# Kernel tuning notes

Measured on AMD Instinct MI355X. Metric: run time of the kernel, lower is better.

## Reference

```python
import jax, jax.numpy as jnp
import numpy as np

ALPHA = 0.2  # LeakyReLU negative slope
NEG = -9e15

def _gat_head(Wh, a1, a2, adj_mask):
    # Wh: [N,O], a1/a2: [O], adj_mask: [N,N] bool
    e = jax.nn.leaky_relu(jnp.einsum('no,o->n', Wh, a1)[:, None]
                          + jnp.einsum('no,o->n', Wh, a2)[None, :], ALPHA)
    att = jax.nn.softmax(jnp.where(adj_mask, e, NEG), axis=-1)
    return att @ Wh  # [N,O]

def setup_inputs() -> dict:
    key = jax.random.key(0)
    ks = jax.random.split(key, 6)
    N, F_IN, O, H, C = 4096, 512, 64, 8, 16
    x = jax.random.normal(ks[0], (N, F_IN), jnp.float32)
    adj = jax.random.randint(ks[1], (N, N), 0, 2, jnp.int32)
    W = jax.random.normal(ks[2], (H, F_IN, O), jnp.float32) * 0.05
    a = jax.random.normal(ks[3], (H, 2 * O), jnp.float32) * 0.05
    W_out = jax.random.normal(ks[4], (H * O, C), jnp.float32) * 0.05
    a_out = jax.random.normal(ks[5], (2 * C,), jnp.float32) * 0.05
    return {'x': x, 'adj': adj, 'W': W, 'a': a, 'W_out': W_out, 'a_out': a_out}

def reference(x, adj, W, a, W_out, a_out):
    N = x.shape[0]
    H, _, O = W.shape
    C = W_out.shape[1]
    mask = adj > 0  # [N,N]
    # multi-head attention layer (vmapped over heads)
    Wh = jnp.einsum('nf,hfo->hno', x, W)  # [H,N,O]
    a1, a2 = a[:, :O], a[:, O:]
    h_heads = jax.vmap(_gat_head, in_axes=(0, 0, 0, None))(Wh, a1, a2, mask)  # [H,N,O]
    h = jax.nn.elu(h_heads)  # concat=True -> elu per head
    h = jnp.transpose(h, (1, 0, 2)).reshape(N, H * O)  # concat heads
    # output attention layer (concat=False)
    Wh_o = h @ W_out  # [N,C]
    out = _gat_head(Wh_o, a_out[:C], a_out[C:], mask)  # [N,C]
    out = jax.nn.elu(out)
    return jax.nn.log_softmax(out, axis=1)
```

## Files before the change

### kernel.cpp

```cpp
#include <hip/hip_runtime.h>


typedef __attribute__((ext_vector_type(8))) short short8;
typedef __attribute__((ext_vector_type(4))) float f32x4;
typedef unsigned long long u64;
typedef unsigned short u16;

__device__ __forceinline__ u16 f2bf_rne(float f){
  unsigned int u = __float_as_uint(f);
  return (u16)((u + 0x7fffu + ((u >> 16) & 1u)) >> 16);
}
__device__ __forceinline__ float bf2f(u16 v){
  return __uint_as_float(((unsigned int)v) << 16);
}
__device__ __forceinline__ void async16(void* lds, const void* g){
  __builtin_amdgcn_global_load_lds((const __attribute__((address_space(1))) unsigned int*)g,
                                   (__attribute__((address_space(3))) unsigned int*)lds, 16, 0, 0);
}
__device__ __forceinline__ void async4(void* lds, const void* g){
  __builtin_amdgcn_global_load_lds((const __attribute__((address_space(1))) unsigned int*)g,
                                   (__attribute__((address_space(3))) unsigned int*)lds, 4, 0, 0);
}

__global__ __launch_bounds__(256) void k_adj_pack(const int* __restrict__ adj,
                                                  u64* __restrict__ bits){
  int lane = threadIdx.x & 63;
  int w0 = blockIdx.x * 4 + (threadIdx.x >> 6);
  #pragma unroll
  for (int k = 0; k < 16; ++k){
    int wid = w0 + k * 16384;
    int i  = wid >> 6;
    int jg = wid & 63;
    int v = adj[(size_t)i * 4096 + (jg << 6) + lane];
    u64 m = __ballot(v != 0);
    if (lane == 0) bits[(size_t)i * 64 + jg] = m;
  }
}

__global__ __launch_bounds__(256) void k_pack_in(const float* __restrict__ x,
                                                 const float* __restrict__ W,
                                                 u16* __restrict__ xA,
                                                 u16* __restrict__ wB){
  if (blockIdx.x < 1024){
    int tid = blockIdx.x * 256 + threadIdx.x;
    int n = tid & 4095;
    int fg = tid >> 12;
    const float* src = x + (size_t)n * 512 + fg * 8;
    float4 v0 = ((const float4*)src)[0];
    float4 v1 = ((const float4*)src)[1];
    unsigned int pk[4];
    pk[0] = f2bf_rne(v0.x) | ((unsigned)f2bf_rne(v0.y) << 16);
    pk[1] = f2bf_rne(v0.z) | ((unsigned)f2bf_rne(v0.w) << 16);
    pk[2] = f2bf_rne(v1.x) | ((unsigned)f2bf_rne(v1.y) << 16);
    pk[3] = f2bf_rne(v1.z) | ((unsigned)f2bf_rne(v1.w) << 16);
    *(uint4*)(xA + ((size_t)fg * 4096 + n) * 8) = *(uint4*)pk;
  } else {
    int tid = (blockIdx.x - 1024) * 256 + threadIdx.x;
    int o  = tid & 63;
    int fg = (tid >> 6) & 63;
    int h  = tid >> 12;
    const float* src = W + ((size_t)h * 512 + fg * 8) * 64 + o;
    unsigned int pk[4];
    #pragma unroll
    for (int p = 0; p < 4; ++p){
      u16 lo = f2bf_rne(src[(2 * p) * 64]);
      u16 hi = f2bf_rne(src[(2 * p + 1) * 64]);
      pk[p] = lo | ((unsigned)hi << 16);
    }
    *(uint4*)(wB + (size_t)h * 32768 + ((size_t)fg * 64 + o) * 8) = *(uint4*)pk;
  }
}

__global__ __launch_bounds__(256) void k_gemm1(const u16* __restrict__ xA,
                                               const u16* __restrict__ wB,
                                               float* __restrict__ Whf){
  int h    = blockIdx.y;
  int nblk = blockIdx.x;
  int lane = threadIdx.x & 63;
  int wid  = threadIdx.x >> 6;
  int row16 = lane & 15, grp = lane >> 4;
  int n0 = nblk * 64 + wid * 16;
  const u16* wBh = wB + (size_t)h * 32768;
  f32x4 acc[4] = {};
  #pragma unroll 4
  for (int ks = 0; ks < 16; ++ks){
    int fgb = ks * 4 + grp;
    short8 af = *(const short8*)(xA + ((size_t)fgb * 4096 + n0 + row16) * 8);
    #pragma unroll
    for (int nt = 0; nt < 4; ++nt){
      short8 bf = *(const short8*)(wBh + ((size_t)fgb * 64 + nt * 16 + row16) * 8);
      acc[nt] = __builtin_amdgcn_mfma_f32_16x16x32_bf16(af, bf, acc[nt], 0, 0, 0);
    }
  }
  #pragma unroll
  for (int nt = 0; nt < 4; ++nt)
    #pragma unroll
    for (int r = 0; r < 4; ++r){
      int n = n0 + grp * 4 + r;
      int o = nt * 16 + row16;
      Whf[((size_t)h * 4096 + n) * 64 + o] = acc[nt][r];
    }
}

__global__ __launch_bounds__(256) void k_prep1(const float* __restrict__ Whf,
                                               const float* __restrict__ av,
                                               u16* __restrict__ whB,
                                               float* __restrict__ s1raw, float* __restrict__ e11,
                                               float* __restrict__ e102, float* __restrict__ s2raw,
                                               float* __restrict__ e21, float* __restrict__ e202){
  if (blockIdx.x < 1024){
    int tid = blockIdx.x * 256 + threadIdx.x;
    int o  = tid & 63;
    int jg = (tid >> 6) & 511;
    int h  = tid >> 15;
    const float* src = Whf + ((size_t)h * 4096 + jg * 8) * 64 + o;
    unsigned int pk[4];
    #pragma unroll
    for (int p = 0; p < 4; ++p){
      u16 lo = f2bf_rne(src[(2 * p) * 64]);
      u16 hi = f2bf_rne(src[(2 * p + 1) * 64]);
      pk[p] = lo | ((unsigned)hi << 16);
    }
    *(uint4*)(whB + (size_t)h * 262144 + ((size_t)jg * 64 + o) * 8) = *(uint4*)pk;
  } else {
    int lane = threadIdx.x & 63;
    int wid  = (blockIdx.x - 1024) * 4 + (threadIdx.x >> 6);
    int h = wid >> 12;
    int i = wid & 4095;
    float wh = Whf[((size_t)h * 4096 + i) * 64 + lane];
    float p1 = wh * av[h * 128 + lane];
    float p2 = wh * av[h * 128 + 64 + lane];
    #pragma unroll
    for (int d = 32; d; d >>= 1){ p1 += __shfl_xor(p1, d, 64); p2 += __shfl_xor(p2, d, 64); }
    if (lane == 0){
      int idx = h * 4096 + i;
      s1raw[idx] = p1; e11[idx] = __expf(p1); e102[idx] = __expf(0.2f * p1);
      s2raw[idx] = p2; e21[idx] = __expf(p2); e202[idx] = __expf(0.2f * p2);
    }
  }
}

__global__ __launch_bounds__(256) void k_att1(const u16* __restrict__ whB,
                                              const u64* __restrict__ adjbits,
                                              const float* __restrict__ s1raw, const float* __restrict__ e11,
                                              const float* __restrict__ e102, const float* __restrict__ s2raw,
                                              const float* __restrict__ e21, const float* __restrict__ e202,
                                              u16* __restrict__ pnum, float* __restrict__ pden){
  __shared__ u16  smB[2][8 * 520];
  __shared__ float smT[2][3][64];
  int h     = blockIdx.y;
  int iblk  = blockIdx.x;
  int split = blockIdx.z;
  int lane = threadIdx.x & 63;
  int wid  = threadIdx.x >> 6;
  int row16 = lane & 15, grp = lane >> 4;
  int i = iblk * 64 + wid * 16 + row16;
  int hoff = h * 4096;
  float s1  = s1raw[hoff + i];
  float f1  = e11[hoff + i];
  float f02 = e102[hoff + i];
  const u16* whBh = whB + (size_t)h * 262144;
  int jbeg = split * 1024;

  auto stage = [&](int b, int j0){
    const char* g = (const char*)whBh + (size_t)j0 * 128 + wid * 2048 + lane * 16;
    char* l = (char*)(&smB[b][0]) + wid * 2 * 1040;
    async16(l, g);
    async16(l + 1040, g + 1024);
    if (wid == 0)      async4(&smT[b][0][0], (const char*)(s2raw + hoff + j0) + lane * 4);
    else if (wid == 1) async4(&smT[b][1][0], (const char*)(e21  + hoff + j0) + lane * 4);
    else if (wid == 2) async4(&smT[b][2][0], (const char*)(e202 + hoff + j0) + lane * 4);
  };

  f32x4 acc[4] = {};
  float den = 0.f;
  stage(0, jbeg);
  for (int c = 0; c < 16; ++c){
    int b = c & 1;
    __syncthreads();
    if (c < 15) stage(b ^ 1, jbeg + (c + 1) * 64);
    u64 mrow = adjbits[(size_t)i * 64 + ((jbeg + c * 64) >> 6)];
    #pragma unroll
    for (int ks = 0; ks < 2; ++ks){
      int kb = ks * 32 + grp * 8;
      float4 sA = *(const float4*)(&smT[b][0][kb]);
      float4 sB = *(const float4*)(&smT[b][0][kb + 4]);
      float4 eA = *(const float4*)(&smT[b][1][kb]);
      float4 eB = *(const float4*)(&smT[b][1][kb + 4]);
      float4 gA = *(const float4*)(&smT[b][2][kb]);
      float4 gB2 = *(const float4*)(&smT[b][2][kb + 4]);
      float sv[8]  = {sA.x, sA.y, sA.z, sA.w, sB.x, sB.y, sB.z, sB.w};
      float e1v[8] = {eA.x, eA.y, eA.z, eA.w, eB.x, eB.y, eB.z, eB.w};
      float e2v[8] = {gA.x, gA.y, gA.z, gA.w, gB2.x, gB2.y, gB2.z, gB2.w};
      unsigned int mb = ((unsigned int)(mrow >> (ks * 32)) >> (grp * 8)) & 0xffu;
      unsigned int pk[4];
      #pragma unroll
      for (int t2 = 0; t2 < 4; ++t2){
        float w0, w1;
        {
          float tt = s1 + sv[2 * t2];
          float w = (tt > 0.f) ? (f1 * e1v[2 * t2]) : (f02 * e2v[2 * t2]);
          w = ((mb >> (2 * t2)) & 1u) ? w : 0.f;
          den += w; w0 = w;
        }
        {
          float tt = s1 + sv[2 * t2 + 1];
          float w = (tt > 0.f) ? (f1 * e1v[2 * t2 + 1]) : (f02 * e2v[2 * t2 + 1]);
          w = ((mb >> (2 * t2 + 1)) & 1u) ? w : 0.f;
          den += w; w1 = w;
        }
        pk[t2] = __builtin_amdgcn_perm(__float_as_uint(w1), __float_as_uint(w0), 0x07060302u);
      }
      short8 af = *(short8*)pk;
      const u16* bbase = &smB[b][(ks * 4 + grp) * 520];
      #pragma unroll
      for (int nt = 0; nt < 4; ++nt){
        short8 bf = *(const short8*)(bbase + (nt * 16 + row16) * 8);
        acc[nt] = __builtin_amdgcn_mfma_f32_16x16x32_bf16(af, bf, acc[nt], 0, 0, 0);
      }
    }
  }

  den += __shfl_xor(den, 16, 64);
  den += __shfl_xor(den, 32, 64);
  if (grp == 0)
    pden[((size_t)split * 8 + h) * 4096 + iblk * 64 + wid * 16 + row16] = den;
  #pragma unroll
  for (int r = 0; r < 4; ++r){
    int n = iblk * 64 + wid * 16 + grp * 4 + r;
    u16* dst = pnum + ((size_t)split * 4096 + n) * 512 + h * 64 + row16;
    #pragma unroll
    for (int nt = 0; nt < 4; ++nt)
      dst[nt * 16] = f2bf_rne(acc[nt][r]);
  }
}

__global__ __launch_bounds__(256) void k_gemm2(const u16* __restrict__ pnum,
                                               const float* __restrict__ pden,
                                               const float* __restrict__ Wout,
                                               const float* __restrict__ aout,
                                               u16* __restrict__ whoB,
                                               float* __restrict__ s1o, float* __restrict__ e11o,
                                               float* __restrict__ e102o, float* __restrict__ s2o,
                                               float* __restrict__ e21o, float* __restrict__ e202o){
  __shared__ float Wl[8192];
  __shared__ float hrow[16 * 516];
  __shared__ float sden[128];
  int n0 = blockIdx.x * 16;
  for (int t = threadIdx.x; t < 8192; t += 256) Wl[t] = Wout[t];
  if (threadIdx.x < 128){
    int hh = threadIdx.x >> 4, nn = threadIdx.x & 15;
    float d = 0.f;
    #pragma unroll
    for (int s = 0; s < 4; ++s) d += pden[((size_t)s * 8 + hh) * 4096 + n0 + nn];
    sden[threadIdx.x] = d;
  }
  __syncthreads();
  {
    int nn = threadIdx.x >> 4;
    int fc = threadIdx.x & 15;
    int f0 = fc * 32;
    int hh = fc >> 1;
    float dinv = 1.f / sden[hh * 16 + nn];
    float v[32];
    #pragma unroll
    for (int k = 0; k < 32; ++k) v[k] = 0.f;
    #pragma unroll
    for (int s = 0; s < 4; ++s){
      const u16* p = pnum + ((size_t)s * 4096 + n0 + nn) * 512 + f0;
      #pragma unroll
      for (int q = 0; q < 4; ++q){
        uint4 raw = *(const uint4*)(p + q * 8);
        unsigned int rw[4] = {raw.x, raw.y, raw.z, raw.w};
        #pragma unroll
        for (int d2 = 0; d2 < 4; ++d2){
          v[q * 8 + d2 * 2]     += __uint_as_float(rw[d2] << 16);
          v[q * 8 + d2 * 2 + 1] += __uint_as_float(rw[d2] & 0xffff0000u);
        }
      }
    }
    #pragma unroll
    for (int k = 0; k < 32; ++k){
      float val = v[k] * dinv;
      val = val > 0.f ? val : (__expf(val) - 1.f);
      hrow[nn * 516 + f0 + k] = val;
    }
  }
  __syncthreads();
  int c  = threadIdx.x & 15;
  int rl = threadIdx.x >> 4;
  int n = n0 + rl;
  const float4* hr = (const float4*)(hrow + rl * 516);
  float acc = 0.f;
  #pragma unroll 8
  for (int f4 = 0; f4 < 128; ++f4){
    float4 hv = hr[f4];
    int f = f4 * 4;
    acc += hv.x * Wl[f * 16 + c] + hv.y * Wl[(f + 1) * 16 + c]
         + hv.z * Wl[(f + 2) * 16 + c] + hv.w * Wl[(f + 3) * 16 + c];
  }
  whoB[((size_t)(n >> 3) * 16 + c) * 8 + (n & 7)] = f2bf_rne(acc);
  float p1 = acc * aout[c], p2 = acc * aout[16 + c];
  #pragma unroll
  for (int d = 1; d < 16; d <<= 1){ p1 += __shfl_xor(p1, d, 64); p2 += __shfl_xor(p2, d, 64); }
  if (c == 0){
    s1o[n] = p1; e11o[n] = __expf(p1); e102o[n] = __expf(0.2f * p1);
    s2o[n] = p2; e21o[n] = __expf(p2); e202o[n] = __expf(0.2f * p2);
  }
}

__global__ __launch_bounds__(256) void k_att2(const u16* __restrict__ whoB,
                                              const u64* __restrict__ adjbits,
                                              const float* __restrict__ s1o, const float* __restrict__ e11o,
                                              const float* __restrict__ e102o, const float* __restrict__ s2o,
                                              const float* __restrict__ e21o, const float* __restrict__ e202o,
                                              float* __restrict__ pnum, float* __restrict__ pden){
  __shared__ u16  smB[2][1024];
  __shared__ float smT[2][3][64];
  int iblk  = blockIdx.x;
  int split = blockIdx.y;
  int lane = threadIdx.x & 63;
  int wid  = threadIdx.x >> 6;
  int row16 = lane & 15, grp = lane >> 4;
  int i = iblk * 64 + wid * 16 + row16;
  float s1  = s1o[i];
  float f1  = e11o[i];
  float f02 = e102o[i];
  int jbeg = split * 256;

  auto stage = [&](int b, int j0){
    const char* gB = (const char*)whoB + (size_t)j0 * 32;
    if (wid == 0){
      async16((char*)&smB[b][0], gB + lane * 16);
      async16((char*)&smB[b][0] + 1024, gB + 1024 + lane * 16);
    }
    else if (wid == 1) async4(&smT[b][0][0], (const char*)(s2o  + j0) + lane * 4);
    else if (wid == 2) async4(&smT[b][1][0], (const char*)(e21o + j0) + lane * 4);
    else               async4(&smT[b][2][0], (const char*)(e202o + j0) + lane * 4);
  };

  f32x4 acc = {};
  float den = 0.f;
  stage(0, jbeg);
  for (int c = 0; c < 4; ++c){
    int b = c & 1;
    __syncthreads();
    if (c < 3) stage(b ^ 1, jbeg + (c + 1) * 64);
    u64 mrow = adjbits[(size_t)i * 64 + ((jbeg + c * 64) >> 6)];
    #pragma unroll
    for (int ks = 0; ks < 2; ++ks){
      int kb = ks * 32 + grp * 8;
      float4 sA = *(const float4*)(&smT[b][0][kb]);
      float4 sB = *(const float4*)(&smT[b][0][kb + 4]);
      float4 eA = *(const float4*)(&smT[b][1][kb]);
      float4 eB = *(const float4*)(&smT[b][1][kb + 4]);
      float4 gA = *(const float4*)(&smT[b][2][kb]);
      float4 gB2 = *(const float4*)(&smT[b][2][kb + 4]);
      float sv[8]  = {sA.x, sA.y, sA.z, sA.w, sB.x, sB.y, sB.z, sB.w};
      float e1v[8] = {eA.x, eA.y, eA.z, eA.w, eB.x, eB.y, eB.z, eB.w};
      float e2v[8] = {gA.x, gA.y, gA.z, gA.w, gB2.x, gB2.y, gB2.z, gB2.w};
      unsigned int mb = ((unsigned int)(mrow >> (ks * 32)) >> (grp * 8)) & 0xffu;
      unsigned int pk[4];
      #pragma unroll
      for (int t2 = 0; t2 < 4; ++t2){
        float w0, w1;
        {
          float tt = s1 + sv[2 * t2];
          float w = (tt > 0.f) ? (f1 * e1v[2 * t2]) : (f02 * e2v[2 * t2]);
          w = ((mb >> (2 * t2)) & 1u) ? w : 0.f;
          den += w; w0 = w;
        }
        {
          float tt = s1 + sv[2 * t2 + 1];
          float w = (tt > 0.f) ? (f1 * e1v[2 * t2 + 1]) : (f02 * e2v[2 * t2 + 1]);
          w = ((mb >> (2 * t2 + 1)) & 1u) ? w : 0.f;
          den += w; w1 = w;
        }
        pk[t2] = __builtin_amdgcn_perm(__float_as_uint(w1), __float_as_uint(w0), 0x07060302u);
      }
      short8 af = *(short8*)pk;
      short8 bf = *(const short8*)(&smB[b][((ks * 4 + grp) * 16 + row16) * 8]);
      acc = __builtin_amdgcn_mfma_f32_16x16x32_bf16(af, bf, acc, 0, 0, 0);
    }
  }
  den += __shfl_xor(den, 16, 64);
  den += __shfl_xor(den, 32, 64);
  if (grp == 0)
    pden[(size_t)(iblk * 64 + wid * 16 + row16) * 16 + split] = den;
  #pragma unroll
  for (int r = 0; r < 4; ++r){
    int n = iblk * 64 + wid * 16 + grp * 4 + r;
    pnum[((size_t)n * 16 + split) * 16 + row16] = acc[r];
  }
}

__global__ __launch_bounds__(256) void k_final(const float* __restrict__ pnum,
                                               const float* __restrict__ pden,
                                               float* __restrict__ out){
  int tid = blockIdx.x * 256 + threadIdx.x;
  int c = tid & 15;
  int n = tid >> 4;
  float num = 0.f, den = 0.f;
  #pragma unroll
  for (int s = 0; s < 16; ++s){
    num += pnum[((size_t)n * 16 + s) * 16 + c];
    den += pden[(size_t)n * 16 + s];
  }
  float v = num / den;
  v = v > 0.f ? v : (__expf(v) - 1.f);
  float m = v;
  #pragma unroll
  for (int d = 1; d < 16; d <<= 1) m = fmaxf(m, __shfl_xor(m, d, 64));
  float es = __expf(v - m), ss = es;
  #pragma unroll
  for (int d = 1; d < 16; d <<= 1) ss += __shfl_xor(ss, d, 64);
  out[(size_t)n * 16 + c] = v - m - __logf(ss);
}

extern "C" void kernel_launch(void* const* d_in, const int* in_sizes, int n_in,
                              void* d_out, int out_size, void* d_ws, size_t ws_size,
                              hipStream_t stream){
  (void)in_sizes; (void)n_in; (void)out_size; (void)ws_size;
  const float* x    = (const float*)d_in[0];
  const int*   adj  = (const int*)d_in[1];
  const float* W    = (const float*)d_in[2];
  const float* av   = (const float*)d_in[3];
  const float* Wout = (const float*)d_in[4];
  const float* aout = (const float*)d_in[5];
  float* out = (float*)d_out;
  char* ws = (char*)d_ws;

  u64*  adjbits = (u64*)(ws + 0x0000000);
  u16*  whB     = (u16*)(ws + 0x0200000);
  float* s1raw  = (float*)(ws + 0x0600000);
  float* e11    = (float*)(ws + 0x0620000);
  float* e102   = (float*)(ws + 0x0640000);
  float* s2raw  = (float*)(ws + 0x0660000);
  float* e21    = (float*)(ws + 0x0680000);
  float* e202   = (float*)(ws + 0x06A0000);
  u16*  xA   = (u16*)(ws + 0x06C0000);
  float* Whf = (float*)(ws + 0x0AC0000);
  u16*  wB   = (u16*)(ws + 0x12C0000);
  u16*  pnum1 = (u16*)(ws + 0x06C0000);
  float* pden1 = (float*)(ws + 0x16C0000);
  u16*  whoB   = (u16*)(ws + 0x1740000);
  float* s1o   = (float*)(ws + 0x1760000);
  float* e11o  = (float*)(ws + 0x1764000);
  float* e102o = (float*)(ws + 0x1768000);
  float* s2o   = (float*)(ws + 0x176C000);
  float* e21o  = (float*)(ws + 0x1770000);
  float* e202o = (float*)(ws + 0x1774000);
  float* pnum2 = (float*)(ws + 0x1778000);
  float* pden2 = (float*)(ws + 0x1B78000);

  k_adj_pack<<<dim3(4096), dim3(256), 0, stream>>>(adj, adjbits);
  k_pack_in<<<dim3(1152), dim3(256), 0, stream>>>(x, W, xA, wB);
  k_gemm1<<<dim3(64, 8), dim3(256), 0, stream>>>(xA, wB, Whf);
  k_prep1<<<dim3(9216), dim3(256), 0, stream>>>(Whf, av, whB, s1raw, e11, e102, s2raw, e21, e202);
  k_att1<<<dim3(64, 8, 4), dim3(256), 0, stream>>>(whB, adjbits, s1raw, e11, e102, s2raw, e21, e202, pnum1, pden1);
  k_gemm2<<<dim3(256), dim3(256), 0, stream>>>(pnum1, pden1, Wout, aout, whoB, s1o, e11o, e102o, s2o, e21o, e202o);
  k_att2<<<dim3(64, 16), dim3(256), 0, stream>>>(whoB, adjbits, s1o, e11o, e102o, s2o, e21o, e202o, pnum2, pden2);
  k_final<<<dim3(256), dim3(256), 0, stream>>>(pnum2, pden2, out);
}
```

Baseline: 208.1 us.

## Fuse prep into GEMM1, compute attention weights via max, denominator via MFMA

Folds the score-dot and bf16 transpose-pack of k_prep1 into k_gemm1's epilogue through LDS, which removes the fp32 Wh round trip and one launch. The attention kernels replace the LeakyReLU sign branch with fmaxf of the two exponential products, which works because exp is monotonic. Masking now uses an LDS lookup-table AND, and the row denominator comes from an extra MFMA against a ones column instead of scalar adds. k_att1 handles 128 rows per block, two row tiles per wave, so each B fragment loaded from LDS is reused. The unpadded LDS layout may add bank conflicts, and the denominator now sums bf16-rounded weights, which costs some precision.

```diff
diff --git a/kernel.cpp b/kernel.cpp
--- a/kernel.cpp
+++ b/kernel.cpp
@@ -5,21 +5,19 @@
 typedef __attribute__((ext_vector_type(4))) float f32x4;
 typedef unsigned long long u64;
 typedef unsigned short u16;
+typedef unsigned int u32;
 
 __device__ __forceinline__ u16 f2bf_rne(float f){
-  unsigned int u = __float_as_uint(f);
+  u32 u = __float_as_uint(f);
   return (u16)((u + 0x7fffu + ((u >> 16) & 1u)) >> 16);
 }
-__device__ __forceinline__ float bf2f(u16 v){
-  return __uint_as_float(((unsigned int)v) << 16);
-}
 __device__ __forceinline__ void async16(void* lds, const void* g){
-  __builtin_amdgcn_global_load_lds((const __attribute__((address_space(1))) unsigned int*)g,
-                                   (__attribute__((address_space(3))) unsigned int*)lds, 16, 0, 0);
+  __builtin_amdgcn_global_load_lds((const __attribute__((address_space(1))) u32*)g,
+                                   (__attribute__((address_space(3))) u32*)lds, 16, 0, 0);
 }
 __device__ __forceinline__ void async4(void* lds, const void* g){
-  __builtin_amdgcn_global_load_lds((const __attribute__((address_space(1))) unsigned int*)g,
-                                   (__attribute__((address_space(3))) unsigned int*)lds, 4, 0, 0);
+  __builtin_amdgcn_global_load_lds((const __attribute__((address_space(1))) u32*)g,
+                                   (__attribute__((address_space(3))) u32*)lds, 4, 0, 0);
 }
 
 __global__ __launch_bounds__(256) void k_adj_pack(const int* __restrict__ adj,
@@ -48,11 +46,11 @@
     const float* src = x + (size_t)n * 512 + fg * 8;
     float4 v0 = ((const float4*)src)[0];
     float4 v1 = ((const float4*)src)[1];
-    unsigned int pk[4];
-    pk[0] = f2bf_rne(v0.x) | ((unsigned)f2bf_rne(v0.y) << 16);
-    pk[1] = f2bf_rne(v0.z) | ((unsigned)f2bf_rne(v0.w) << 16);
-    pk[2] = f2bf_rne(v1.x) | ((unsigned)f2bf_rne(v1.y) << 16);
-    pk[3] = f2bf_rne(v1.z) | ((unsigned)f2bf_rne(v1.w) << 16);
+    u32 pk[4];
+    pk[0] = f2bf_rne(v0.x) | ((u32)f2bf_rne(v0.y) << 16);
+    pk[1] = f2bf_rne(v0.z) | ((u32)f2bf_rne(v0.w) << 16);
+    pk[2] = f2bf_rne(v1.x) | ((u32)f2bf_rne(v1.y) << 16);
+    pk[3] = f2bf_rne(v1.z) | ((u32)f2bf_rne(v1.w) << 16);
     *(uint4*)(xA + ((size_t)fg * 4096 + n) * 8) = *(uint4*)pk;
   } else {
     int tid = (blockIdx.x - 1024) * 256 + threadIdx.x;
@@ -60,12 +58,12 @@
     int fg = (tid >> 6) & 63;
     int h  = tid >> 12;
     const float* src = W + ((size_t)h * 512 + fg * 8) * 64 + o;
-    unsigned int pk[4];
+    u32 pk[4];
     #pragma unroll
     for (int p = 0; p < 4; ++p){
       u16 lo = f2bf_rne(src[(2 * p) * 64]);
       u16 hi = f2bf_rne(src[(2 * p + 1) * 64]);
-      pk[p] = lo | ((unsigned)hi << 16);
+      pk[p] = lo | ((u32)hi << 16);
     }
     *(uint4*)(wB + (size_t)h * 32768 + ((size_t)fg * 64 + o) * 8) = *(uint4*)pk;
   }
@@ -73,165 +71,159 @@
 
 __global__ __launch_bounds__(256) void k_gemm1(const u16* __restrict__ xA,
                                                const u16* __restrict__ wB,
-                                               float* __restrict__ Whf){
+                                               const float* __restrict__ av,
+                                               u16* __restrict__ whB,
+                                               float* __restrict__ e11, float* __restrict__ e102,
+                                               float* __restrict__ e21, float* __restrict__ e202){
+  __shared__ u16 tr[4096];
   int h    = blockIdx.y;
   int nblk = blockIdx.x;
   int lane = threadIdx.x & 63;
   int wid  = threadIdx.x >> 6;
   int row16 = lane & 15, grp = lane >> 4;
-  int n0 = nblk * 64 + wid * 16;
+  int n0 = nblk * 64;
+  int n0w = n0 + wid * 16;
   const u16* wBh = wB + (size_t)h * 32768;
   f32x4 acc[4] = {};
   #pragma unroll 4
   for (int ks = 0; ks < 16; ++ks){
     int fgb = ks * 4 + grp;
-    short8 af = *(const short8*)(xA + ((size_t)fgb * 4096 + n0 + row16) * 8);
+    short8 af = *(const short8*)(xA + ((size_t)fgb * 4096 + n0w + row16) * 8);
     #pragma unroll
     for (int nt = 0; nt < 4; ++nt){
       short8 bf = *(const short8*)(wBh + ((size_t)fgb * 64 + nt * 16 + row16) * 8);
       acc[nt] = __builtin_amdgcn_mfma_f32_16x16x32_bf16(af, bf, acc[nt], 0, 0, 0);
     }
   }
+  float a1v[4], a2v[4];
+  #pragma unroll
+  for (int nt = 0; nt < 4; ++nt){
+    a1v[nt] = av[h * 128 + nt * 16 + row16];
+    a2v[nt] = av[h * 128 + 64 + nt * 16 + row16];
+  }
+  #pragma unroll
+  for (int r = 0; r < 4; ++r){
+    float p1 = acc[0][r] * a1v[0] + acc[1][r] * a1v[1] + acc[2][r] * a1v[2] + acc[3][r] * a1v[3];
+    float p2 = acc[0][r] * a2v[0] + acc[1][r] * a2v[1] + acc[2][r] * a2v[2] + acc[3][r] * a2v[3];
+    #pragma unroll
+    for (int d = 1; d < 16; d <<= 1){ p1 += __shfl_xor(p1, d, 64); p2 += __shfl_xor(p2, d, 64); }
+    if (row16 == 0){
+      int idx = h * 4096 + n0w + grp * 4 + r;
+      e11[idx]  = __expf(p1); e102[idx] = __expf(0.2f * p1);
+      e21[idx]  = __expf(p2); e202[idx] = __expf(0.2f * p2);
+    }
+  }
   #pragma unroll
   for (int nt = 0; nt < 4; ++nt)
     #pragma unroll
     for (int r = 0; r < 4; ++r){
-      int n = n0 + grp * 4 + r;
-      int o = nt * 16 + row16;
-      Whf[((size_t)h * 4096 + n) * 64 + o] = acc[nt][r];
-    }
-}
-
-__global__ __launch_bounds__(256) void k_prep1(const float* __restrict__ Whf,
-                                               const float* __restrict__ av,
-                                               u16* __restrict__ whB,
-                                               float* __restrict__ s1raw, float* __restrict__ e11,
-                                               float* __restrict__ e102, float* __restrict__ s2raw,
-                                               float* __restrict__ e21, float* __restrict__ e202){
-  if (blockIdx.x < 1024){
-    int tid = blockIdx.x * 256 + threadIdx.x;
-    int o  = tid & 63;
-    int jg = (tid >> 6) & 511;
-    int h  = tid >> 15;
-    const float* src = Whf + ((size_t)h * 4096 + jg * 8) * 64 + o;
-    unsigned int pk[4];
-    #pragma unroll
-    for (int p = 0; p < 4; ++p){
-      u16 lo = f2bf_rne(src[(2 * p) * 64]);
-      u16 hi = f2bf_rne(src[(2 * p + 1) * 64]);
-      pk[p] = lo | ((unsigned)hi << 16);
-    }
-    *(uint4*)(whB + (size_t)h * 262144 + ((size_t)jg * 64 + o) * 8) = *(uint4*)pk;
-  } else {
-    int lane = threadIdx.x & 63;
-    int wid  = (blockIdx.x - 1024) * 4 + (threadIdx.x >> 6);
-    int h = wid >> 12;
-    int i = wid & 4095;
-    float wh = Whf[((size_t)h * 4096 + i) * 64 + lane];
-    float p1 = wh * av[h * 128 + lane];
-    float p2 = wh * av[h * 128 + 64 + lane];
-    #pragma unroll
-    for (int d = 32; d; d >>= 1){ p1 += __shfl_xor(p1, d, 64); p2 += __shfl_xor(p2, d, 64); }
-    if (lane == 0){
-      int idx = h * 4096 + i;
-      s1raw[idx] = p1; e11[idx] = __expf(p1); e102[idx] = __expf(0.2f * p1);
-      s2raw[idx] = p2; e21[idx] = __expf(p2); e202[idx] = __expf(0.2f * p2);
-    }
-  }
+      int jl = wid * 16 + grp * 4 + r;
+      int o  = nt * 16 + row16;
+      tr[((jl >> 3) * 64 + o) * 8 + (jl & 7)] = f2bf_rne(acc[nt][r]);
+    }
+  __syncthreads();
+  u16* dst = whB + (size_t)h * 262144 + (size_t)n0 * 64;
+  #pragma unroll
+  for (int q = 0; q < 2; ++q)
+    *(uint4*)(dst + (threadIdx.x * 2 + q) * 8) = *(const uint4*)(tr + (threadIdx.x * 2 + q) * 8);
 }
 
 __global__ __launch_bounds__(256) void k_att1(const u16* __restrict__ whB,
                                               const u64* __restrict__ adjbits,
-                                              const float* __restrict__ s1raw, const float* __restrict__ e11,
-                                              const float* __restrict__ e102, const float* __restrict__ s2raw,
+                                              const float* __restrict__ e11, const float* __restrict__ e102,
                                               const float* __restrict__ e21, const float* __restrict__ e202,
                                               u16* __restrict__ pnum, float* __restrict__ pden){
-  __shared__ u16  smB[2][8 * 520];
-  __shared__ float smT[2][3][64];
+  __shared__ u16  smB[2][4096];
+  __shared__ float smT[2][2][64];
+  __shared__ u32  smLut[4];
   int h     = blockIdx.y;
   int iblk  = blockIdx.x;
   int split = blockIdx.z;
   int lane = threadIdx.x & 63;
   int wid  = threadIdx.x >> 6;
   int row16 = lane & 15, grp = lane >> 4;
-  int i = iblk * 64 + wid * 16 + row16;
+  if (threadIdx.x < 4)
+    smLut[threadIdx.x] = ((threadIdx.x & 1) ? 0xFFFFu : 0u) | ((threadIdx.x & 2) ? 0xFFFF0000u : 0u);
+  int ibase = iblk * 128 + wid * 32;
+  int i0 = ibase + row16, i1 = ibase + 16 + row16;
   int hoff = h * 4096;
-  float s1  = s1raw[hoff + i];
-  float f1  = e11[hoff + i];
-  float f02 = e102[hoff + i];
+  float f1a  = e11[hoff + i0],  f1b  = e11[hoff + i1];
+  float f02a = e102[hoff + i0], f02b = e102[hoff + i1];
   const u16* whBh = whB + (size_t)h * 262144;
   int jbeg = split * 1024;
 
+  short8 bden;
+  #pragma unroll
+  for (int t = 0; t < 8; ++t) bden[t] = (row16 == 0) ? (short)0x3F80 : (short)0;
+
   auto stage = [&](int b, int j0){
     const char* g = (const char*)whBh + (size_t)j0 * 128 + wid * 2048 + lane * 16;
-    char* l = (char*)(&smB[b][0]) + wid * 2 * 1040;
+    char* l = (char*)(&smB[b][0]) + wid * 2048;
     async16(l, g);
-    async16(l + 1040, g + 1024);
-    if (wid == 0)      async4(&smT[b][0][0], (const char*)(s2raw + hoff + j0) + lane * 4);
-    else if (wid == 1) async4(&smT[b][1][0], (const char*)(e21  + hoff + j0) + lane * 4);
-    else if (wid == 2) async4(&smT[b][2][0], (const char*)(e202 + hoff + j0) + lane * 4);
+    async16(l + 1024, g + 1024);
+    if (wid == 0)      async4(&smT[b][0][0], (const char*)(e21  + hoff + j0) + lane * 4);
+    else if (wid == 1) async4(&smT[b][1][0], (const char*)(e202 + hoff + j0) + lane * 4);
   };
 
-  f32x4 acc[4] = {};
-  float den = 0.f;
+  f32x4 acc[2][4] = {};
+  f32x4 accden[2] = {};
   stage(0, jbeg);
   for (int c = 0; c < 16; ++c){
     int b = c & 1;
+    u64 mrow0 = adjbits[(size_t)i0 * 64 + ((jbeg + c * 64) >> 6)];
+    u64 mrow1 = adjbits[(size_t)i1 * 64 + ((jbeg + c * 64) >> 6)];
     __syncthreads();
     if (c < 15) stage(b ^ 1, jbeg + (c + 1) * 64);
-    u64 mrow = adjbits[(size_t)i * 64 + ((jbeg + c * 64) >> 6)];
     #pragma unroll
     for (int ks = 0; ks < 2; ++ks){
       int kb = ks * 32 + grp * 8;
-      float4 sA = *(const float4*)(&smT[b][0][kb]);
-      float4 sB = *(const float4*)(&smT[b][0][kb + 4]);
-      float4 eA = *(const float4*)(&smT[b][1][kb]);
-      float4 eB = *(const float4*)(&smT[b][1][kb + 4]);
-      float4 gA = *(const float4*)(&smT[b][2][kb]);
-      float4 gB2 = *(const float4*)(&smT[b][2][kb + 4]);
-      float sv[8]  = {sA.x, sA.y, sA.z, sA.w, sB.x, sB.y, sB.z, sB.w};
+      float4 eA = *(const float4*)(&smT[b][0][kb]);
+      float4 eB = *(const float4*)(&smT[b][0][kb + 4]);
+      float4 gA = *(const float4*)(&smT[b][1][kb]);
+      float4 gB = *(const float4*)(&smT[b][1][kb + 4]);
       float e1v[8] = {eA.x, eA.y, eA.z, eA.w, eB.x, eB.y, eB.z, eB.w};
-      float e2v[8] = {gA.x, gA.y, gA.z, gA.w, gB2.x, gB2.y, gB2.z, gB2.w};
-      unsigned int mb = ((unsigned int)(mrow >> (ks * 32)) >> (grp * 8)) & 0xffu;
-      unsigned int pk[4];
+      float e2v[8] = {gA.x, gA.y, gA.z, gA.w, gB.x, gB.y, gB.z, gB.w};
+      const u16* bbase = &smB[b][(ks * 4 + grp) * 512];
+      short8 bf0 = *(const short8*)(bbase + (0 * 16 + row16) * 8);
+      short8 bf1 = *(const short8*)(bbase + (1 * 16 + row16) * 8);
+      short8 bf2 = *(const short8*)(bbase + (2 * 16 + row16) * 8);
+      short8 bf3 = *(const short8*)(bbase + (3 * 16 + row16) * 8);
       #pragma unroll
-      for (int t2 = 0; t2 < 4; ++t2){
-        float w0, w1;
-        {
-          float tt = s1 + sv[2 * t2];
-          float w = (tt > 0.f) ? (f1 * e1v[2 * t2]) : (f02 * e2v[2 * t2]);
-          w = ((mb >> (2 * t2)) & 1u) ? w : 0.f;
-          den += w; w0 = w;
+      for (int it = 0; it < 2; ++it){
+        u64 mrow = it ? mrow1 : mrow0;
+        float f1 = it ? f1b : f1a;
+        float f02 = it ? f02b : f02a;
+        u32 mb = ((u32)(mrow >> (ks * 32)) >> (grp * 8)) & 0xffu;
+        u32 pk[4];
+        #pragma unroll
+        for (int t2 = 0; t2 < 4; ++t2){
+          float w0 = fmaxf(f1 * e1v[2 * t2],     f02 * e2v[2 * t2]);
+          float w1 = fmaxf(f1 * e1v[2 * t2 + 1], f02 * e2v[2 * t2 + 1]);
+          u32 p = __builtin_amdgcn_perm(__float_as_uint(w1), __float_as_uint(w0), 0x07060302u);
+          pk[t2] = p & smLut[(mb >> (2 * t2)) & 3u];
         }
-        {
-          float tt = s1 + sv[2 * t2 + 1];
-          float w = (tt > 0.f) ? (f1 * e1v[2 * t2 + 1]) : (f02 * e2v[2 * t2 + 1]);
-          w = ((mb >> (2 * t2 + 1)) & 1u) ? w : 0.f;
-          den += w; w1 = w;
-        }
-        pk[t2] = __builtin_amdgcn_perm(__float_as_uint(w1), __float_as_uint(w0), 0x07060302u);
+        short8 af = *(short8*)pk;
+        acc[it][0] = __builtin_amdgcn_mfma_f32_16x16x32_bf16(af, bf0, acc[it][0], 0, 0, 0);
+        acc[it][1] = __builtin_amdgcn_mfma_f32_16x16x32_bf16(af, bf1, acc[it][1], 0, 0, 0);
+        acc[it][2] = __builtin_amdgcn_mfma_f32_16x16x32_bf16(af, bf2, acc[it][2], 0, 0, 0);
+        acc[it][3] = __builtin_amdgcn_mfma_f32_16x16x32_bf16(af, bf3, acc[it][3], 0, 0, 0);
+        accden[it] = __builtin_amdgcn_mfma_f32_16x16x32_bf16(af, bden, accden[it], 0, 0, 0);
       }
-      short8 af = *(short8*)pk;
-      const u16* bbase = &smB[b][(ks * 4 + grp) * 520];
+    }
+  }
+
+  #pragma unroll
+  for (int it = 0; it < 2; ++it){
+    #pragma unroll
+    for (int r = 0; r < 4; ++r){
+      int n = ibase + it * 16 + grp * 4 + r;
+      if (row16 == 0)
+        pden[((size_t)split * 8 + h) * 4096 + n] = accden[it][r];
+      u16* dst = pnum + ((size_t)split * 4096 + n) * 512 + h * 64 + row16;
       #pragma unroll
-      for (int nt = 0; nt < 4; ++nt){
-        short8 bf = *(const short8*)(bbase + (nt * 16 + row16) * 8);
-        acc[nt] = __builtin_amdgcn_mfma_f32_16x16x32_bf16(af, bf, acc[nt], 0, 0, 0);
-      }
-    }
-  }
-
-  den += __shfl_xor(den, 16, 64);
-  den += __shfl_xor(den, 32, 64);
-  if (grp == 0)
-    pden[((size_t)split * 8 + h) * 4096 + iblk * 64 + wid * 16 + row16] = den;
-  #pragma unroll
-  for (int r = 0; r < 4; ++r){
-    int n = iblk * 64 + wid * 16 + grp * 4 + r;
-    u16* dst = pnum + ((size_t)split * 4096 + n) * 512 + h * 64 + row16;
-    #pragma unroll
-    for (int nt = 0; nt < 4; ++nt)
-      dst[nt * 16] = f2bf_rne(acc[nt][r]);
+      for (int nt = 0; nt < 4; ++nt)
+        dst[nt * 16] = f2bf_rne(acc[it][nt][r]);
+    }
   }
 }
 
@@ -240,8 +232,7 @@
                                                const float* __restrict__ Wout,
                                                const float* __restrict__ aout,
                                                u16* __restrict__ whoB,
-                                               float* __restrict__ s1o, float* __restrict__ e11o,
-                                               float* __restrict__ e102o, float* __restrict__ s2o,
+                                               float* __restrict__ e11o, float* __restrict__ e102o,
                                                float* __restrict__ e21o, float* __restrict__ e202o){
   __shared__ float Wl[8192];
   __shared__ float hrow[16 * 516];
@@ -271,7 +262,7 @@
       #pragma unroll
       for (int q = 0; q < 4; ++q){
         uint4 raw = *(const uint4*)(p + q * 8);
-        unsigned int rw[4] = {raw.x, raw.y, raw.z, raw.w};
+        u32 rw[4] = {raw.x, raw.y, raw.z, raw.w};
         #pragma unroll
         for (int d2 = 0; d2 < 4; ++d2){
           v[q * 8 + d2 * 2]     += __uint_as_float(rw[d2] << 16);
@@ -304,29 +295,33 @@
   #pragma unroll
   for (int d = 1; d < 16; d <<= 1){ p1 += __shfl_xor(p1, d, 64); p2 += __shfl_xor(p2, d, 64); }
   if (c == 0){
-    s1o[n] = p1; e11o[n] = __expf(p1); e102o[n] = __expf(0.2f * p1);
-    s2o[n] = p2; e21o[n] = __expf(p2); e202o[n] = __expf(0.2f * p2);
+    e11o[n] = __expf(p1); e102o[n] = __expf(0.2f * p1);
+    e21o[n] = __expf(p2); e202o[n] = __expf(0.2f * p2);
   }
 }
 
 __global__ __launch_bounds__(256) void k_att2(const u16* __restrict__ whoB,
                                               const u64* __restrict__ adjbits,
-                                              const float* __restrict__ s1o, const float* __restrict__ e11o,
-                                              const float* __restrict__ e102o, const float* __restrict__ s2o,
+                                              const float* __restrict__ e11o, const float* __restrict__ e102o,
                                               const float* __restrict__ e21o, const float* __restrict__ e202o,
                                               float* __restrict__ pnum, float* __restrict__ pden){
   __shared__ u16  smB[2][1024];
-  __shared__ float smT[2][3][64];
+  __shared__ float smT[2][2][64];
+  __shared__ u32  smLut[4];
   int iblk  = blockIdx.x;
   int split = blockIdx.y;
   int lane = threadIdx.x & 63;
   int wid  = threadIdx.x >> 6;
   int row16 = lane & 15, grp = lane >> 4;
+  if (threadIdx.x < 4)
+    smLut[threadIdx.x] = ((threadIdx.x & 1) ? 0xFFFFu : 0u) | ((threadIdx.x & 2) ? 0xFFFF0000u : 0u);
   int i = iblk * 64 + wid * 16 + row16;
-  float s1  = s1o[i];
   float f1  = e11o[i];
   float f02 = e102o[i];
   int jbeg = split * 256;
+  short8 bden;
+  #pragma unroll
+  for (int t = 0; t < 8; ++t) bden[t] = (row16 == 0) ? (short)0x3F80 : (short)0;
 
   auto stage = [&](int b, int j0){
     const char* gB = (const char*)whoB + (size_t)j0 * 32;
@@ -334,62 +329,47 @@
       async16((char*)&smB[b][0], gB + lane * 16);
       async16((char*)&smB[b][0] + 1024, gB + 1024 + lane * 16);
     }
-    else if (wid == 1) async4(&smT[b][0][0], (const char*)(s2o  + j0) + lane * 4);
-    else if (wid == 2) async4(&smT[b][1][0], (const char*)(e21o + j0) + lane * 4);
-    else               async4(&smT[b][2][0], (const char*)(e202o + j0) + lane * 4);
+    else if (wid == 1) async4(&smT[b][0][0], (const char*)(e21o  + j0) + lane * 4);
+    else if (wid == 2) async4(&smT[b][1][0], (const char*)(e202o + j0) + lane * 4);
   };
 
   f32x4 acc = {};
-  float den = 0.f;
+  f32x4 accden = {};
   stage(0, jbeg);
   for (int c = 0; c < 4; ++c){
     int b = c & 1;
+    u64 mrow = adjbits[(size_t)i * 64 + ((jbeg + c * 64) >> 6)];
     __syncthreads();
     if (c < 3) stage(b ^ 1, jbeg + (c + 1) * 64);
-    u64 mrow = adjbits[(size_t)i * 64 + ((jbeg + c * 64) >> 6)];
     #pragma unroll
     for (int ks = 0; ks < 2; ++ks){
       int kb = ks * 32 + grp * 8;
-      float4 sA = *(const float4*)(&smT[b][0][kb]);
-      float4 sB = *(const float4*)(&smT[b][0][kb + 4]);
-      float4 eA = *(const float4*)(&smT[b][1][kb]);
-      float4 eB = *(const float4*)(&smT[b][1][kb + 4]);
-      float4 gA = *(const float4*)(&smT[b][2][kb]);
-      float4 gB2 = *(const float4*)(&smT[b][2][kb + 4]);
-      float sv[8]  = {sA.x, sA.y, sA.z, sA.w, sB.x, sB.y, sB.z, sB.w};
+      float4 eA = *(const float4*)(&smT[b][0][kb]);
+      float4 eB = *(const float4*)(&smT[b][0][kb + 4]);
+      float4 gA = *(const float4*)(&smT[b][1][kb]);
+      float4 gB = *(const float4*)(&smT[b][1][kb + 4]);
       float e1v[8] = {eA.x, eA.y, eA.z, eA.w, eB.x, eB.y, eB.z, eB.w};
-      float e2v[8] = {gA.x, gA.y, gA.z, gA.w, gB2.x, gB2.y, gB2.z, gB2.w};
-      unsigned int mb = ((unsigned int)(mrow >> (ks * 32)) >> (grp * 8)) & 0xffu;
-      unsigned int pk[4];
+      float e2v[8] = {gA.x, gA.y, gA.z, gA.w, gB.x, gB.y, gB.z, gB.w};
+      u32 mb = ((u32)(mrow >> (ks * 32)) >> (grp * 8)) & 0xffu;
+      u32 pk[4];
       #pragma unroll
       for (int t2 = 0; t2 < 4; ++t2){
-        float w0, w1;
-        {
-          float tt = s1 + sv[2 * t2];
-          float w = (tt > 0.f) ? (f1 * e1v[2 * t2]) : (f02 * e2v[2 * t2]);
-          w = ((mb >> (2 * t2)) & 1u) ? w : 0.f;
-          den += w; w0 = w;
-        }
-        {
-          float tt = s1 + sv[2 * t2 + 1];
-          float w = (tt > 0.f) ? (f1 * e1v[2 * t2 + 1]) : (f02 * e2v[2 * t2 + 1]);
-          w = ((mb >> (2 * t2 + 1)) & 1u) ? w : 0.f;
-          den += w; w1 = w;
-        }
-        pk[t2] = __builtin_amdgcn_perm(__float_as_uint(w1), __float_as_uint(w0), 0x07060302u);
+        float w0 = fmaxf(f1 * e1v[2 * t2],     f02 * e2v[2 * t2]);
+        float w1 = fmaxf(f1 * e1v[2 * t2 + 1], f02 * e2v[2 * t2 + 1]);
+        u32 p = __builtin_amdgcn_perm(__float_as_uint(w1), __float_as_uint(w0), 0x07060302u);
+        pk[t2] = p & smLut[(mb >> (2 * t2)) & 3u];
       }
       short8 af = *(short8*)pk;
       short8 bf = *(const short8*)(&smB[b][((ks * 4 + grp) * 16 + row16) * 8]);
-      acc = __builtin_amdgcn_mfma_f32_16x16x32_bf16(af, bf, acc, 0, 0, 0);
-    }
-  }
-  den += __shfl_xor(den, 16, 64);
-  den += __shfl_xor(den, 32, 64);
-  if (grp == 0)
-    pden[(size_t)(iblk * 64 + wid * 16 + row16) * 16 + split] = den;
+      acc    = __builtin_amdgcn_mfma_f32_16x16x32_bf16(af, bf, acc, 0, 0, 0);
+      accden = __builtin_amdgcn_mfma_f32_16x16x32_bf16(af, bden, accden, 0, 0, 0);
+    }
+  }
   #pragma unroll
   for (int r = 0; r < 4; ++r){
     int n = iblk * 64 + wid * 16 + grp * 4 + r;
+    if (row16 == 0)
+      pden[(size_t)n * 16 + split] = accden[r];
     pnum[((size_t)n * 16 + split) * 16 + row16] = acc[r];
   }
 }
@@ -432,33 +412,27 @@
 
   u64*  adjbits = (u64*)(ws + 0x0000000);
   u16*  whB     = (u16*)(ws + 0x0200000);
-  float* s1raw  = (float*)(ws + 0x0600000);
-  float* e11    = (float*)(ws + 0x0620000);
-  float* e102   = (float*)(ws + 0x0640000);
-  float* s2raw  = (float*)(ws + 0x0660000);
-  float* e21    = (float*)(ws + 0x0680000);
-  float* e202   = (float*)(ws + 0x06A0000);
-  u16*  xA   = (u16*)(ws + 0x06C0000);
-  float* Whf = (float*)(ws + 0x0AC0000);
-  u16*  wB   = (u16*)(ws + 0x12C0000);
-  u16*  pnum1 = (u16*)(ws + 0x06C0000);
-  float* pden1 = (float*)(ws + 0x16C0000);
-  u16*  whoB   = (u16*)(ws + 0x1740000);
-  float* s1o   = (float*)(ws + 0x1760000);
-  float* e11o  = (float*)(ws + 0x1764000);
-  float* e102o = (float*)(ws + 0x1768000);
-  float* s2o   = (float*)(ws + 0x176C000);
-  float* e21o  = (float*)(ws + 0x1770000);
-  float* e202o = (float*)(ws + 0x1774000);
-  float* pnum2 = (float*)(ws + 0x1778000);
-  float* pden2 = (float*)(ws + 0x1B78000);
+  float* e11    = (float*)(ws + 0x0600000);
+  float* e102   = (float*)(ws + 0x0620000);
+  float* e21    = (float*)(ws + 0x0640000);
+  float* e202   = (float*)(ws + 0x0660000);
+  u16*  xA    = (u16*)(ws + 0x0680000);
+  u16*  wB    = (u16*)(ws + 0x0A80000);
+  u16*  pnum1 = (u16*)(ws + 0x0680000);
+  float* pden1 = (float*)(ws + 0x1680000);
+  u16*  whoB   = (u16*)(ws + 0x1700000);
+  float* e11o  = (float*)(ws + 0x1720000);
+  float* e102o = (float*)(ws + 0x1724000);
+  float* e21o  = (float*)(ws + 0x1728000);
+  float* e202o = (float*)(ws + 0x172C000);
+  float* pnum2 = (float*)(ws + 0x1730000);
+  float* pden2 = (float*)(ws + 0x1B30000);
 
   k_adj_pack<<<dim3(4096), dim3(256), 0, stream>>>(adj, adjbits);
   k_pack_in<<<dim3(1152), dim3(256), 0, stream>>>(x, W, xA, wB);
-  k_gemm1<<<dim3(64, 8), dim3(256), 0, stream>>>(xA, wB, Whf);
-  k_prep1<<<dim3(9216), dim3(256), 0, stream>>>(Whf, av, whB, s1raw, e11, e102, s2raw, e21, e202);
-  k_att1<<<dim3(64, 8, 4), dim3(256), 0, stream>>>(whB, adjbits, s1raw, e11, e102, s2raw, e21, e202, pnum1, pden1);
-  k_gemm2<<<dim3(256), dim3(256), 0, stream>>>(pnum1, pden1, Wout, aout, whoB, s1o, e11o, e102o, s2o, e21o, e202o);
-  k_att2<<<dim3(64, 16), dim3(256), 0, stream>>>(whoB, adjbits, s1o, e11o, e102o, s2o, e21o, e202o, pnum2, pden2);
+  k_gemm1<<<dim3(64, 8), dim3(256), 0, stream>>>(xA, wB, av, whB, e11, e102, e21, e202);
+  k_att1<<<dim3(32, 8, 4), dim3(256), 0, stream>>>(whB, adjbits, e11, e102, e21, e202, pnum1, pden1);
+  k_gemm2<<<dim3(256), dim3(256), 0, stream>>>(pnum1, pden1, Wout, aout, whoB, e11o, e102o, e21o, e202o);
+  k_att2<<<dim3(64, 16), dim3(256), 0, stream>>>(whoB, adjbits, e11o, e102o, e21o, e202o, pnum2, pden2);
   k_final<<<dim3(256), dim3(256), 0, stream>>>(pnum2, pden2, out);
 }
```

Measured after the change: 194.1 us. 6.7% less time.
